# Optimization experiments

Hardware: AMD Instinct MI355X
Metric: run time of the kernel (lower is better)

The kernel has to match this reference:

```python
import jax, jax.numpy as jnp
import numpy as np

EPS = 1e-12  # torch F.normalize eps

def l2norm(x, axis=-1):
    n = jnp.linalg.norm(x, axis=axis, keepdims=True)
    return x / jnp.maximum(n, EPS)

def setup_inputs() -> dict:
    key = jax.random.key(0)
    ks = jax.random.split(key, 8)
    n_vocab, d, n_asp = 100000, 256, 14
    B, L, M = 512, 100, 10
    pos = jax.random.randint(ks[0], (B, L), 0, n_vocab)
    negs = jax.random.randint(ks[1], (B, M, L), 0, n_vocab)
    E_w = jax.random.normal(ks[2], (n_vocab, d), dtype=jnp.float32) * 0.1
    T_w = jax.random.normal(ks[3], (n_asp, d), dtype=jnp.float32) * 0.1
    M_w = jax.random.uniform(ks[4], (d, d), dtype=jnp.float32, minval=-0.1, maxval=0.1)
    M_b = jnp.zeros((d,), dtype=jnp.float32)
    lin_w = jax.random.normal(ks[5], (n_asp, d), dtype=jnp.float32) * 0.05
    lin_b = jnp.zeros((n_asp,), dtype=jnp.float32)
    return {"pos": pos, "negs": negs, "E_w": E_w, "T_w": T_w,
            "M_w": M_w, "M_b": M_b, "lin_w": lin_w, "lin_b": lin_b}

def reference(pos, negs, E_w, T_w, M_w, M_b, lin_w, lin_b):
    # e: [B, L, d] (original keeps e_i as [B, d, L]; layout differs, math identical)
    e = E_w[pos]
    y_s = jnp.mean(e, axis=1)                    # mean over tokens -> [B, d]
    My = y_s @ M_w.T + M_b                       # [B, d]
    d_i = jnp.tanh(jnp.einsum('bld,bd->bl', e, My))  # [B, L]
    # NOTE: original normalizes exp(d_i) by the GLOBAL sum over the whole batch
    a_i = jnp.exp(d_i) / jnp.sum(jnp.exp(d_i))   # [B, L]
    z_s = l2norm(jnp.einsum('bld,bl->bd', e, a_i))   # [B, d]
    p_t = jax.nn.softmax(z_s @ lin_w.T + lin_b, axis=1)  # [B, n_asp]
    r_s = l2norm(p_t @ T_w)                      # [B, d]
    e_n = E_w[negs]                              # [B, M, L, d]
    z_n = l2norm(jnp.mean(e_n, axis=2))          # [B, M, d]
    return (r_s, z_s, z_n)
```

## Files before the change

### kernel.cpp

```cpp
#include <hip/hip_runtime.h>
#include <math.h>

#define D 256

__device__ __forceinline__ float wave_reduce_sum(float v) {
#pragma unroll
    for (int off = 32; off > 0; off >>= 1) v += __shfl_xor(v, off);
    return v;
}

__global__ __launch_bounds__(256) void abae_main_kernel(
    const int* __restrict__ pos, const float* __restrict__ E_w,
    const float* __restrict__ T_w, const float* __restrict__ M_w,
    const float* __restrict__ M_b, const float* __restrict__ lin_w,
    const float* __restrict__ lin_b, float* __restrict__ r_s,
    float* __restrict__ z_s, int L, int n_asp) {
    const int b    = blockIdx.x;
    const int t    = threadIdx.x;
    const int lane = t & 63;
    const int wv   = t >> 6;
    const int* __restrict__ posb = pos + (size_t)b * L;

    __shared__ float  sy[D];
    __shared__ float  smy[D];
    __shared__ float4 sred[4][64];
    __shared__ float  slog[16];
    __shared__ float  sp[16];
    __shared__ float  sscal[4];

    float4 acc = make_float4(0.f, 0.f, 0.f, 0.f);
    for (int l = wv; l < L; l += 4) {
        const int idx = posb[l];
        const float4 e4 = ((const float4*)(E_w + (size_t)idx * D))[lane];
        acc.x += e4.x; acc.y += e4.y; acc.z += e4.z; acc.w += e4.w;
    }
    sred[wv][lane] = acc;
    __syncthreads();
    if (wv == 0) {
        float4 y  = sred[0][lane];
        const float4 a1 = sred[1][lane], a2 = sred[2][lane], a3 = sred[3][lane];
        const float invL = 1.f / (float)L;
        y.x = (y.x + a1.x + a2.x + a3.x) * invL;
        y.y = (y.y + a1.y + a2.y + a3.y) * invL;
        y.z = (y.z + a1.z + a2.z + a3.z) * invL;
        y.w = (y.w + a1.w + a2.w + a3.w) * invL;
        ((float4*)sy)[lane] = y;
    }
    __syncthreads();

    float m = M_b[t];
    const float4* __restrict__ mwrow = (const float4*)(M_w + (size_t)t * D);
#pragma unroll 8
    for (int k = 0; k < D / 4; ++k) {
        const float4 v = mwrow[k];
        m += sy[4 * k + 0] * v.x + sy[4 * k + 1] * v.y +
             sy[4 * k + 2] * v.z + sy[4 * k + 3] * v.w;
    }
    smy[t] = m;
    __syncthreads();

    const float4 my4 = ((const float4*)smy)[lane];
    float4 zacc = make_float4(0.f, 0.f, 0.f, 0.f);
    for (int l = wv; l < L; l += 4) {
        const int idx = posb[l];
        const float4 e4 = ((const float4*)(E_w + (size_t)idx * D))[lane];
        float p = e4.x * my4.x + e4.y * my4.y + e4.z * my4.z + e4.w * my4.w;
        p = wave_reduce_sum(p);
        const float w = expf(tanhf(p));
        zacc.x += e4.x * w; zacc.y += e4.y * w;
        zacc.z += e4.z * w; zacc.w += e4.w * w;
    }
    sred[wv][lane] = zacc;
    __syncthreads();
    if (wv == 0) {
        float4 z  = sred[0][lane];
        const float4 a1 = sred[1][lane], a2 = sred[2][lane], a3 = sred[3][lane];
        z.x += a1.x + a2.x + a3.x;
        z.y += a1.y + a2.y + a3.y;
        z.z += a1.z + a2.z + a3.z;
        z.w += a1.w + a2.w + a3.w;
        float ss = z.x * z.x + z.y * z.y + z.z * z.z + z.w * z.w;
        ss = wave_reduce_sum(ss);
        const float inv = 1.f / fmaxf(sqrtf(ss), 1e-12f);
        z.x *= inv; z.y *= inv; z.z *= inv; z.w *= inv;
        ((float4*)(z_s + (size_t)b * D))[lane] = z;
        ((float4*)sy)[lane] = z;
    }
    __syncthreads();

    const float4 z4 = ((const float4*)sy)[lane];
    for (int a = wv; a < n_asp; a += 4) {
        const float4 w4 = ((const float4*)(lin_w + (size_t)a * D))[lane];
        float p = z4.x * w4.x + z4.y * w4.y + z4.z * w4.z + z4.w * w4.w;
        p = wave_reduce_sum(p);
        if (lane == 0) slog[a] = p + lin_b[a];
    }
    __syncthreads();
    if (t == 0) {
        float mx = -1e30f;
        for (int a = 0; a < n_asp; ++a) mx = fmaxf(mx, slog[a]);
        float s = 0.f;
        for (int a = 0; a < n_asp; ++a) {
            const float e = expf(slog[a] - mx);
            sp[a] = e; s += e;
        }
        const float invs = 1.f / s;
        for (int a = 0; a < n_asp; ++a) sp[a] *= invs;
    }
    __syncthreads();

    float r = 0.f;
    for (int a = 0; a < n_asp; ++a) r += sp[a] * T_w[(size_t)a * D + t];
    float sq = wave_reduce_sum(r * r);
    if (lane == 0) sscal[wv] = sq;
    __syncthreads();
    const float tot = sscal[0] + sscal[1] + sscal[2] + sscal[3];
    const float inv = 1.f / fmaxf(sqrtf(tot), 1e-12f);
    r_s[(size_t)b * D + t] = r * inv;
}

__global__ __launch_bounds__(256) void abae_negs_kernel(
    const int* __restrict__ negs, const float* __restrict__ E_w,
    float* __restrict__ z_n, int L) {
    const int bm   = blockIdx.x;
    const int t    = threadIdx.x;
    const int lane = t & 63;
    const int wv   = t >> 6;
    const int* __restrict__ idxp = negs + (size_t)bm * L;

    float4 acc = make_float4(0.f, 0.f, 0.f, 0.f);
    for (int l = wv; l < L; l += 4) {
        const int idx = idxp[l];
        const float4 e4 = ((const float4*)(E_w + (size_t)idx * D))[lane];
        acc.x += e4.x; acc.y += e4.y; acc.z += e4.z; acc.w += e4.w;
    }
    __shared__ float4 sred[4][64];
    sred[wv][lane] = acc;
    __syncthreads();
    if (wv == 0) {
        float4 z  = sred[0][lane];
        const float4 a1 = sred[1][lane], a2 = sred[2][lane], a3 = sred[3][lane];
        const float invL = 1.f / (float)L;
        z.x = (z.x + a1.x + a2.x + a3.x) * invL;
        z.y = (z.y + a1.y + a2.y + a3.y) * invL;
        z.z = (z.z + a1.z + a2.z + a3.z) * invL;
        z.w = (z.w + a1.w + a2.w + a3.w) * invL;
        float ss = z.x * z.x + z.y * z.y + z.z * z.z + z.w * z.w;
        ss = wave_reduce_sum(ss);
        const float inv = 1.f / fmaxf(sqrtf(ss), 1e-12f);
        z.x *= inv; z.y *= inv; z.z *= inv; z.w *= inv;
        ((float4*)(z_n + (size_t)bm * D))[lane] = z;
    }
}

extern "C" void kernel_launch(void* const* d_in, const int* in_sizes, int n_in,
                              void* d_out, int out_size, void* d_ws, size_t ws_size,
                              hipStream_t stream) {
    const int*   pos   = (const int*)d_in[0];
    const int*   negs  = (const int*)d_in[1];
    const float* E_w   = (const float*)d_in[2];
    const float* T_w   = (const float*)d_in[3];
    const float* M_w   = (const float*)d_in[4];
    const float* M_b   = (const float*)d_in[5];
    const float* lin_w = (const float*)d_in[6];
    const float* lin_b = (const float*)d_in[7];
    float* out = (float*)d_out;

    const int d     = in_sizes[5];
    const int n_asp = in_sizes[7];
    const int M     = in_sizes[1] / in_sizes[0];
    const int B     = out_size / (d * (2 + M));
    const int L     = in_sizes[0] / B;
    (void)d; (void)n_in; (void)d_ws; (void)ws_size;

    float* r_s = out;
    float* z_s = out + (size_t)B * d;
    float* z_n = out + (size_t)2 * B * d;

    abae_negs_kernel<<<B * M, 256, 0, stream>>>(negs, E_w, z_n, L);
    abae_main_kernel<<<B, 256, 0, stream>>>(pos, E_w, T_w, M_w, M_b, lin_w,
                                            lin_b, r_s, z_s, L, n_asp);
}
```

Baseline: 267.0 us.

## Cache gathered embeddings in LDS and unroll gather loads for more parallelism

The main kernel now stores each batch row's gathered embedding rows in a 100 KB shared-memory buffer during the mean pass. The attention pass reads them from LDS instead of gathering from global memory a second time. The block grows to 512 threads and each wave takes a contiguous chunk of tokens with 4-way unrolled loads. The negatives kernel also uses contiguous chunks with 5-way unrolled independent gathers to raise memory-level parallelism. The trade-offs are a hard-coded LMAX=100 limit and large LDS use, which cuts blocks per CU.

```diff
diff --git a/kernel.cpp b/kernel.cpp
--- a/kernel.cpp
+++ b/kernel.cpp
@@ -2,6 +2,7 @@
 #include <math.h>
 
 #define D 256
+#define LMAX 100
 
 __device__ __forceinline__ float wave_reduce_sum(float v) {
 #pragma unroll
@@ -9,7 +10,7 @@
     return v;
 }
 
-__global__ __launch_bounds__(256) void abae_main_kernel(
+__global__ __launch_bounds__(512) void abae_main_kernel(
     const int* __restrict__ pos, const float* __restrict__ E_w,
     const float* __restrict__ T_w, const float* __restrict__ M_w,
     const float* __restrict__ M_b, const float* __restrict__ lin_w,
@@ -19,66 +20,109 @@
     const int t    = threadIdx.x;
     const int lane = t & 63;
     const int wv   = t >> 6;
+    const int NW   = 8;
     const int* __restrict__ posb = pos + (size_t)b * L;
 
+    __shared__ float  se[LMAX * D];
     __shared__ float  sy[D];
     __shared__ float  smy[D];
-    __shared__ float4 sred[4][64];
+    __shared__ float4 sred[8][64];
     __shared__ float  slog[16];
     __shared__ float  sp[16];
-    __shared__ float  sscal[4];
+    __shared__ float  sscal[8];
+
+    const int C  = (L + NW - 1) / NW;
+    const int s0 = wv * C;
+    const int e0 = min(L, s0 + C);
 
     float4 acc = make_float4(0.f, 0.f, 0.f, 0.f);
-    for (int l = wv; l < L; l += 4) {
+    int l = s0;
+    for (; l + 3 < e0; l += 4) {
+        const int i0 = posb[l], i1 = posb[l + 1], i2 = posb[l + 2], i3 = posb[l + 3];
+        const float4 a0 = ((const float4*)(E_w + (size_t)i0 * D))[lane];
+        const float4 a1 = ((const float4*)(E_w + (size_t)i1 * D))[lane];
+        const float4 a2 = ((const float4*)(E_w + (size_t)i2 * D))[lane];
+        const float4 a3 = ((const float4*)(E_w + (size_t)i3 * D))[lane];
+        ((float4*)se)[(l + 0) * 64 + lane] = a0;
+        ((float4*)se)[(l + 1) * 64 + lane] = a1;
+        ((float4*)se)[(l + 2) * 64 + lane] = a2;
+        ((float4*)se)[(l + 3) * 64 + lane] = a3;
+        acc.x += a0.x + a1.x + a2.x + a3.x;
+        acc.y += a0.y + a1.y + a2.y + a3.y;
+        acc.z += a0.z + a1.z + a2.z + a3.z;
+        acc.w += a0.w + a1.w + a2.w + a3.w;
+    }
+    for (; l < e0; ++l) {
         const int idx = posb[l];
-        const float4 e4 = ((const float4*)(E_w + (size_t)idx * D))[lane];
-        acc.x += e4.x; acc.y += e4.y; acc.z += e4.z; acc.w += e4.w;
+        const float4 a0 = ((const float4*)(E_w + (size_t)idx * D))[lane];
+        ((float4*)se)[l * 64 + lane] = a0;
+        acc.x += a0.x; acc.y += a0.y; acc.z += a0.z; acc.w += a0.w;
     }
     sred[wv][lane] = acc;
     __syncthreads();
     if (wv == 0) {
-        float4 y  = sred[0][lane];
-        const float4 a1 = sred[1][lane], a2 = sred[2][lane], a3 = sred[3][lane];
+        float4 y = sred[0][lane];
+#pragma unroll
+        for (int w = 1; w < 8; ++w) {
+            const float4 a = sred[w][lane];
+            y.x += a.x; y.y += a.y; y.z += a.z; y.w += a.w;
+        }
         const float invL = 1.f / (float)L;
-        y.x = (y.x + a1.x + a2.x + a3.x) * invL;
-        y.y = (y.y + a1.y + a2.y + a3.y) * invL;
-        y.z = (y.z + a1.z + a2.z + a3.z) * invL;
-        y.w = (y.w + a1.w + a2.w + a3.w) * invL;
+        y.x *= invL; y.y *= invL; y.z *= invL; y.w *= invL;
         ((float4*)sy)[lane] = y;
     }
     __syncthreads();
 
-    float m = M_b[t];
-    const float4* __restrict__ mwrow = (const float4*)(M_w + (size_t)t * D);
+    if (t < D) {
+        float m = M_b[t];
+        const float4* __restrict__ mwrow = (const float4*)(M_w + (size_t)t * D);
 #pragma unroll 8
-    for (int k = 0; k < D / 4; ++k) {
-        const float4 v = mwrow[k];
-        m += sy[4 * k + 0] * v.x + sy[4 * k + 1] * v.y +
-             sy[4 * k + 2] * v.z + sy[4 * k + 3] * v.w;
-    }
-    smy[t] = m;
+        for (int k = 0; k < D / 4; ++k) {
+            const float4 v = mwrow[k];
+            m += sy[4 * k + 0] * v.x + sy[4 * k + 1] * v.y +
+                 sy[4 * k + 2] * v.z + sy[4 * k + 3] * v.w;
+        }
+        smy[t] = m;
+    }
     __syncthreads();
 
     const float4 my4 = ((const float4*)smy)[lane];
     float4 zacc = make_float4(0.f, 0.f, 0.f, 0.f);
-    for (int l = wv; l < L; l += 4) {
-        const int idx = posb[l];
-        const float4 e4 = ((const float4*)(E_w + (size_t)idx * D))[lane];
-        float p = e4.x * my4.x + e4.y * my4.y + e4.z * my4.z + e4.w * my4.w;
-        p = wave_reduce_sum(p);
-        const float w = expf(tanhf(p));
-        zacc.x += e4.x * w; zacc.y += e4.y * w;
-        zacc.z += e4.z * w; zacc.w += e4.w * w;
+    l = s0;
+    for (; l + 1 < e0; l += 2) {
+        const float4 ea = ((const float4*)se)[(l + 0) * 64 + lane];
+        const float4 eb = ((const float4*)se)[(l + 1) * 64 + lane];
+        float pa = ea.x * my4.x + ea.y * my4.y + ea.z * my4.z + ea.w * my4.w;
+        float pb = eb.x * my4.x + eb.y * my4.y + eb.z * my4.z + eb.w * my4.w;
+#pragma unroll
+        for (int off = 32; off > 0; off >>= 1) {
+            pa += __shfl_xor(pa, off);
+            pb += __shfl_xor(pb, off);
+        }
+        const float wa = expf(tanhf(pa));
+        const float wb = expf(tanhf(pb));
+        zacc.x += ea.x * wa + eb.x * wb;
+        zacc.y += ea.y * wa + eb.y * wb;
+        zacc.z += ea.z * wa + eb.z * wb;
+        zacc.w += ea.w * wa + eb.w * wb;
+    }
+    for (; l < e0; ++l) {
+        const float4 ea = ((const float4*)se)[l * 64 + lane];
+        float pa = ea.x * my4.x + ea.y * my4.y + ea.z * my4.z + ea.w * my4.w;
+        pa = wave_reduce_sum(pa);
+        const float wa = expf(tanhf(pa));
+        zacc.x += ea.x * wa; zacc.y += ea.y * wa;
+        zacc.z += ea.z * wa; zacc.w += ea.w * wa;
     }
     sred[wv][lane] = zacc;
     __syncthreads();
     if (wv == 0) {
-        float4 z  = sred[0][lane];
-        const float4 a1 = sred[1][lane], a2 = sred[2][lane], a3 = sred[3][lane];
-        z.x += a1.x + a2.x + a3.x;
-        z.y += a1.y + a2.y + a3.y;
-        z.z += a1.z + a2.z + a3.z;
-        z.w += a1.w + a2.w + a3.w;
+        float4 z = sred[0][lane];
+#pragma unroll
+        for (int w = 1; w < 8; ++w) {
+            const float4 a = sred[w][lane];
+            z.x += a.x; z.y += a.y; z.z += a.z; z.w += a.w;
+        }
         float ss = z.x * z.x + z.y * z.y + z.z * z.z + z.w * z.w;
         ss = wave_reduce_sum(ss);
         const float inv = 1.f / fmaxf(sqrtf(ss), 1e-12f);
@@ -89,7 +133,7 @@
     __syncthreads();
 
     const float4 z4 = ((const float4*)sy)[lane];
-    for (int a = wv; a < n_asp; a += 4) {
+    for (int a = wv; a < n_asp; a += NW) {
         const float4 w4 = ((const float4*)(lin_w + (size_t)a * D))[lane];
         float p = z4.x * w4.x + z4.y * w4.y + z4.z * w4.z + z4.w * w4.w;
         p = wave_reduce_sum(p);
@@ -110,13 +154,17 @@
     __syncthreads();
 
     float r = 0.f;
-    for (int a = 0; a < n_asp; ++a) r += sp[a] * T_w[(size_t)a * D + t];
+    if (t < D) {
+        for (int a = 0; a < n_asp; ++a) r += sp[a] * T_w[(size_t)a * D + t];
+    }
     float sq = wave_reduce_sum(r * r);
     if (lane == 0) sscal[wv] = sq;
     __syncthreads();
-    const float tot = sscal[0] + sscal[1] + sscal[2] + sscal[3];
-    const float inv = 1.f / fmaxf(sqrtf(tot), 1e-12f);
-    r_s[(size_t)b * D + t] = r * inv;
+    if (t < D) {
+        const float tot = sscal[0] + sscal[1] + sscal[2] + sscal[3];
+        const float inv = 1.f / fmaxf(sqrtf(tot), 1e-12f);
+        r_s[(size_t)b * D + t] = r * inv;
+    }
 }
 
 __global__ __launch_bounds__(256) void abae_negs_kernel(
@@ -128,12 +176,31 @@
     const int wv   = t >> 6;
     const int* __restrict__ idxp = negs + (size_t)bm * L;
 
+    const int C  = (L + 3) / 4;
+    const int s0 = wv * C;
+    const int e0 = min(L, s0 + C);
+
     float4 acc = make_float4(0.f, 0.f, 0.f, 0.f);
-    for (int l = wv; l < L; l += 4) {
+    int l = s0;
+    for (; l + 5 <= e0; l += 5) {
+        const int i0 = idxp[l], i1 = idxp[l + 1], i2 = idxp[l + 2],
+                  i3 = idxp[l + 3], i4 = idxp[l + 4];
+        const float4 v0 = ((const float4*)(E_w + (size_t)i0 * D))[lane];
+        const float4 v1 = ((const float4*)(E_w + (size_t)i1 * D))[lane];
+        const float4 v2 = ((const float4*)(E_w + (size_t)i2 * D))[lane];
+        const float4 v3 = ((const float4*)(E_w + (size_t)i3 * D))[lane];
+        const float4 v4 = ((const float4*)(E_w + (size_t)i4 * D))[lane];
+        acc.x += v0.x + v1.x + v2.x + v3.x + v4.x;
+        acc.y += v0.y + v1.y + v2.y + v3.y + v4.y;
+        acc.z += v0.z + v1.z + v2.z + v3.z + v4.z;
+        acc.w += v0.w + v1.w + v2.w + v3.w + v4.w;
+    }
+    for (; l < e0; ++l) {
         const int idx = idxp[l];
-        const float4 e4 = ((const float4*)(E_w + (size_t)idx * D))[lane];
-        acc.x += e4.x; acc.y += e4.y; acc.z += e4.z; acc.w += e4.w;
-    }
+        const float4 v = ((const float4*)(E_w + (size_t)idx * D))[lane];
+        acc.x += v.x; acc.y += v.y; acc.z += v.z; acc.w += v.w;
+    }
+
     __shared__ float4 sred[4][64];
     sred[wv][lane] = acc;
     __syncthreads();
@@ -178,6 +245,6 @@
     float* z_n = out + (size_t)2 * B * d;
 
     abae_negs_kernel<<<B * M, 256, 0, stream>>>(negs, E_w, z_n, L);
-    abae_main_kernel<<<B, 256, 0, stream>>>(pos, E_w, T_w, M_w, M_b, lin_w,
+    abae_main_kernel<<<B, 512, 0, stream>>>(pos, E_w, T_w, M_w, M_b, lin_w,
                                             lin_b, r_s, z_s, L, n_asp);
 }
```

New measurement: 253.0 us. -5.2%, faster.
